# Optimization experiments

Measured on AMD Instinct MI355X. Metric: run time of the kernel, lower is better.

## Reference

```python
import jax, jax.numpy as jnp
import numpy as np

N_HEAD = 8
D_MODEL = 128  # per-head dim == d_model in this 'interpretable' MHA
B, S = 2, 2048
LN_EPS = 1e-3  # keras LayerNormalization default epsilon


def setup_inputs() -> dict:
    key = jax.random.key(0)
    ks = jax.random.split(key, 8)
    sc = 1.0 / np.sqrt(D_MODEL)
    q = jax.random.normal(ks[0], (B, S, D_MODEL), jnp.float32)
    k = jax.random.normal(ks[1], (B, S, D_MODEL), jnp.float32)
    v = jax.random.normal(ks[2], (B, S, D_MODEL), jnp.float32)
    # multiplicative causal mask (lower-triangular ones), broadcast over B,H
    mask = jnp.tril(jnp.ones((S, S), jnp.float32))[None, None, :, :]
    Wq = jax.random.normal(ks[3], (D_MODEL, N_HEAD * D_MODEL), jnp.float32) * sc
    Wk = jax.random.normal(ks[4], (D_MODEL, N_HEAD * D_MODEL), jnp.float32) * sc
    Wv = jax.random.normal(ks[5], (D_MODEL, N_HEAD * D_MODEL), jnp.float32) * sc
    Wo = jax.random.normal(ks[6], (N_HEAD * D_MODEL, D_MODEL), jnp.float32) * sc
    gamma = jnp.ones((D_MODEL,), jnp.float32)
    beta = jnp.zeros((D_MODEL,), jnp.float32)
    return {"q": q, "k": k, "v": v, "mask": mask, "Wq": Wq, "Wk": Wk,
            "Wv": Wv, "Wo": Wo, "gamma": gamma, "beta": beta}


def reference(q, k, v, mask, Wq, Wk, Wv, Wo, gamma, beta):
    b = q.shape[0]
    # projections -> [B, H, S, D]
    def split_heads(x):
        return x.reshape(b, -1, N_HEAD, D_MODEL).transpose(0, 2, 1, 3)
    qs = split_heads(q @ Wq)
    ks_ = split_heads(k @ Wk)
    vs = split_heads(v @ Wv)
    scores = jnp.einsum('bhqd,bhkd->bhqk', qs, ks_) / jnp.sqrt(jnp.float32(D_MODEL))
    scores = scores * mask  # multiplicative mask (NOT additive -inf)
    attn = jax.nn.softmax(scores, axis=-1)
    # dropout layers are identity at inference
    out = jnp.einsum('bhqk,bhkd->bhqd', attn, vs)
    out = out.transpose(0, 2, 1, 3).reshape(b, -1, N_HEAD * D_MODEL)
    out = out @ Wo
    # keras LayerNorm (axis=-1, eps=1e-3)
    mu = jnp.mean(out, axis=-1, keepdims=True)
    var = jnp.var(out, axis=-1, keepdims=True)
    out = (out - mu) * jax.lax.rsqrt(var + LN_EPS) * gamma + beta
    return out
```

## Files before the change

### kernel.cpp

```cpp
#include <hip/hip_runtime.h>
#include <math.h>

#define B 2
#define S 2048
#define H 8
#define D 128
#define DM 1024
#define BH 16

typedef unsigned short u16;
typedef __attribute__((ext_vector_type(8))) short bf16x8;
typedef __attribute__((ext_vector_type(8))) unsigned short u16x8;
typedef __attribute__((ext_vector_type(4))) float f32x4;

__device__ __forceinline__ float bf2f(u16 x) {
    union { unsigned u; float f; } c; c.u = ((unsigned)x) << 16; return c.f;
}
__device__ __forceinline__ u16 f2bf(float f) {
    union { unsigned u; float f; } c; c.f = f;
    unsigned u = c.u; u += 0x7fffu + ((u >> 16) & 1u);
    return (u16)(u >> 16);
}
__device__ __forceinline__ u16 ftr(float f) {
    union { unsigned u; float f; } c; c.f = f;
    return (u16)(c.u >> 16);
}

#define MFMA16(a, b, c) __builtin_amdgcn_mfma_f32_16x16x32_bf16((a), (b), (c), 0, 0, 0)

__global__ __launch_bounds__(256) void prep_kernel(
    const float* __restrict__ Wq, const float* __restrict__ Wk, const float* __restrict__ Wv,
    const float* __restrict__ Wo, u16* __restrict__ WT, u16* __restrict__ WoT)
{
    __shared__ __align__(16) u16 Wl[128][132];
    int tid = threadIdx.x, by = blockIdx.x;
    if (by < 16) {
        int k0 = by * 64;
#pragma unroll
        for (int i = 0; i < 8; i++) {
            int e = i * 256 + tid; int kk = e >> 5, n4 = e & 31;
            float4 w4 = *(const float4*)&Wo[(size_t)(k0 + kk) * D + n4 * 4];
            ushort4 p; p.x = ftr(w4.x); p.y = ftr(w4.y); p.z = ftr(w4.z); p.w = ftr(w4.w);
            *(ushort4*)&Wl[kk][n4 * 4] = p;
        }
        __syncthreads();
#pragma unroll
        for (int i = 0; i < 4; i++) {
            int e = i * 256 + tid; int n = e >> 3, ko = e & 7;
            u16x8 g;
#pragma unroll
            for (int j = 0; j < 8; j++) g[j] = Wl[ko * 8 + j][n];
            *(u16x8*)&WoT[(size_t)n * DM + k0 + ko * 8] = g;
        }
    } else {
        int tile = by - 16;
        int t = tile >> 3, h = tile & 7;
        const float* W = (t == 0) ? Wq : (t == 1) ? Wk : Wv;
        int col0 = h * 128;
#pragma unroll
        for (int i = 0; i < 16; i++) {
            int e = i * 256 + tid; int kk = e >> 5, n4 = e & 31;
            float4 w4 = *(const float4*)&W[(size_t)kk * DM + col0 + n4 * 4];
            ushort4 p; p.x = ftr(w4.x); p.y = ftr(w4.y); p.z = ftr(w4.z); p.w = ftr(w4.w);
            *(ushort4*)&Wl[kk][n4 * 4] = p;
        }
        __syncthreads();
        u16* WTt = WT + (size_t)tile * (128 * 128);
#pragma unroll
        for (int i = 0; i < 8; i++) {
            int e = i * 256 + tid; int n = e >> 4, ko = e & 15;
            u16x8 g;
#pragma unroll
            for (int j = 0; j < 8; j++) g[j] = Wl[ko * 8 + j][n];
            *(u16x8*)&WTt[(size_t)n * 128 + ko * 8] = g;
        }
    }
}

__global__ __launch_bounds__(256) void proj_kernel(
    const float* __restrict__ q, const float* __restrict__ k, const float* __restrict__ v,
    const u16* __restrict__ WT,
    u16* __restrict__ Qo, u16* __restrict__ Ko, u16* __restrict__ VTo,
    float* __restrict__ Csum)
{
    __shared__ __align__(16) u16 Xs[64][136];
    __shared__ __align__(16) u16 Ws[128][136];
    int tid = threadIdx.x;
    int m0 = blockIdx.x * 64;
    int by = blockIdx.y;
    int t = by >> 3;
    int h = by & 7;
    const float* X = (t == 0) ? q : (t == 1) ? k : v;
    const u16* WTt = WT + (size_t)(t * 8 + h) * (128 * 128);

#pragma unroll
    for (int i = 0; i < 8; i++) {
        int e = i * 256 + tid; int r = e >> 5, c4 = e & 31;
        float4 x4 = *(const float4*)&X[(size_t)(m0 + r) * D + c4 * 4];
        ushort4 p; p.x = ftr(x4.x); p.y = ftr(x4.y); p.z = ftr(x4.z); p.w = ftr(x4.w);
        *(ushort4*)&Xs[r][c4 * 4] = p;
    }
#pragma unroll
    for (int i = 0; i < 8; i++) {
        int e = i * 256 + tid; int n = e >> 4, c8 = e & 15;
        *(u16x8*)&Ws[n][c8 * 8] = *(const u16x8*)&WTt[(size_t)n * 128 + c8 * 8];
    }
    __syncthreads();

    int w = tid >> 6, lane = tid & 63, quad = lane >> 4, ln = lane & 15;
    bf16x8 aX[4];
#pragma unroll
    for (int ks = 0; ks < 4; ks++)
        aX[ks] = *(const bf16x8*)&Xs[w * 16 + ln][ks * 32 + quad * 8];

    f32x4 zero = {0.f, 0.f, 0.f, 0.f};
    f32x4 acc[8];
#pragma unroll
    for (int nt = 0; nt < 8; nt++) acc[nt] = zero;

#pragma unroll
    for (int ks = 0; ks < 4; ks++) {
        bf16x8 bW[8];
#pragma unroll
        for (int nt = 0; nt < 8; nt++)
            bW[nt] = *(const bf16x8*)&Ws[nt * 16 + ln][ks * 32 + quad * 8];
#pragma unroll
        for (int nt = 0; nt < 8; nt++)
            acc[nt] = MFMA16(aX[ks], bW[nt], acc[nt]);
    }

    int bb = m0 >> 11, ss0 = m0 & 2047;
    int bh = bb * 8 + h;
    __syncthreads();
    if (t < 2) {
        u16 (*Ct)[136] = Xs;
        u16* O = (t == 0) ? Qo : Ko;
#pragma unroll
        for (int nt = 0; nt < 8; nt++)
#pragma unroll
            for (int r = 0; r < 4; r++)
                Ct[w * 16 + quad * 4 + r][nt * 16 + ln] = f2bf(acc[nt][r]);
        __syncthreads();
#pragma unroll
        for (int i = 0; i < 4; i++) {
            int e = i * 256 + tid; int r = e >> 4, c8 = e & 15;
            *(u16x8*)&O[((size_t)bh * S + ss0 + r) * D + c8 * 8] = *(const u16x8*)&Ct[r][c8 * 8];
        }
    } else {
        u16 (*Ct)[68] = (u16 (*)[68])&Xs[0][0];
#pragma unroll
        for (int nt = 0; nt < 8; nt++)
#pragma unroll
            for (int r = 0; r < 4; r++)
                Ct[nt * 16 + ln][w * 16 + quad * 4 + r] = f2bf(acc[nt][r]);
        __syncthreads();
#pragma unroll
        for (int i = 0; i < 4; i++) {
            int e = i * 256 + tid; int dloc = e >> 3, c8 = e & 7;
            *(u16x8*)&VTo[((size_t)bh * D + dloc) * S + ss0 + c8 * 8] =
                *(const u16x8*)&Ct[dloc][c8 * 8];
        }
        if (tid < 128) {
            int d = tid;
            float s = 0.f;
#pragma unroll
            for (int i = 0; i < 8; i++) {
                u16x8 v8 = *(const u16x8*)&Ct[d][i * 8];
#pragma unroll
                for (int j = 0; j < 8; j++) s += bf2f(v8[j]);
            }
            Csum[((size_t)bh * 32 + (ss0 >> 6)) * D + d] = s;
        }
    }
}

__global__ __launch_bounds__(256, 3) void attn_kernel(
    const u16* __restrict__ Qb, const u16* __restrict__ Kb, const u16* __restrict__ VTg,
    const float* __restrict__ Csum, u16* __restrict__ HOb)
{
    __shared__ __align__(16) u16 Qs[64][136];
    __shared__ __align__(16) u16 Ps[64][72];
    __shared__ __align__(16) u16 Vt[128][72];
    __shared__ float Lred[4][64];

    int tid = threadIdx.x;
    int bh = blockIdx.x;
    int y  = blockIdx.y;
    int qb = (y < 16) ? (31 - y) : (y - 16);
    int q0 = qb * 64;
    int ntile = qb + 1;
    int w = tid >> 6, lane = tid & 63, quad = lane >> 4, ln = lane & 15;
    const u16* Qp  = Qb  + (size_t)bh * S * D;
    const u16* Kp  = Kb  + (size_t)bh * S * D;
    const u16* VTp = VTg + (size_t)bh * D * S;

#pragma unroll
    for (int i = 0; i < 4; i++) {
        int e = i * 256 + tid; int r = e >> 4, c8 = e & 15;
        *(u16x8*)&Qs[r][c8 * 8] = *(const u16x8*)&Qp[(size_t)(q0 + r) * D + c8 * 8];
    }
#pragma unroll
    for (int i = 0; i < 4; i++) {
        int e = i * 256 + tid; int dd = e >> 3, c8 = e & 7;
        *(u16x8*)&Vt[dd][c8 * 8] = *(const u16x8*)&VTp[(size_t)dd * S + c8 * 8];
    }
    bf16x8 kfrag[4];
#pragma unroll
    for (int ks = 0; ks < 4; ks++)
        kfrag[ks] = *(const bf16x8*)&Kp[(size_t)(w * 16 + ln) * D + ks * 32 + quad * 8];
    __syncthreads();

    f32x4 zero = {0.f, 0.f, 0.f, 0.f};
    f32x4 accPV[4][2], acc_l[4];
#pragma unroll
    for (int rf = 0; rf < 4; rf++) { accPV[rf][0] = zero; accPV[rf][1] = zero; acc_l[rf] = zero; }
    bf16x8 bOnes;
#pragma unroll
    for (int j = 0; j < 8; j++) bOnes[j] = (short)0x3F80;
    const float scale = 0.08838834764831845f;

    bf16x8 kn[4];
    u16x8 vreg[4];
    for (int kt = 0; kt < ntile; kt++) {
        int k1 = (kt + 1) * 64;
        bool pf = (kt + 1 < ntile);
        if (pf) {
#pragma unroll
            for (int ks = 0; ks < 4; ks++)
                kn[ks] = *(const bf16x8*)&Kp[(size_t)(k1 + w * 16 + ln) * D + ks * 32 + quad * 8];
#pragma unroll
            for (int i = 0; i < 4; i++) {
                int e = i * 256 + tid; int dd = e >> 3, c8 = e & 7;
                vreg[i] = *(const u16x8*)&VTp[(size_t)dd * S + k1 + c8 * 8];
            }
        }
        f32x4 s[4];
#pragma unroll
        for (int rf = 0; rf < 4; rf++) s[rf] = zero;
        __builtin_amdgcn_s_setprio(1);
#pragma unroll
        for (int ks = 0; ks < 4; ks++) {
#pragma unroll
            for (int rf = 0; rf < 4; rf++) {
                bf16x8 aQ = *(const bf16x8*)&Qs[rf * 16 + ln][ks * 32 + quad * 8];
                s[rf] = MFMA16(aQ, kfrag[ks], s[rf]);
            }
        }
        __builtin_amdgcn_s_setprio(0);
        int colb = kt * 64 + w * 16 + ln;
        if (kt == qb) {
#pragma unroll
            for (int rf = 0; rf < 4; rf++) {
                int rowb = q0 + rf * 16 + quad * 4;
#pragma unroll
                for (int r = 0; r < 4; r++) {
                    float tv = (colb <= rowb + r) ? s[rf][r] : 0.f;
                    Ps[rf * 16 + quad * 4 + r][w * 16 + ln] = f2bf(__expf(tv * scale));
                }
            }
        } else {
#pragma unroll
            for (int rf = 0; rf < 4; rf++)
#pragma unroll
                for (int r = 0; r < 4; r++)
                    Ps[rf * 16 + quad * 4 + r][w * 16 + ln] = f2bf(__expf(s[rf][r] * scale));
        }
        __syncthreads();
        __builtin_amdgcn_s_setprio(1);
#pragma unroll
        for (int ks = 0; ks < 2; ks++) {
            bf16x8 aP[4];
#pragma unroll
            for (int rf = 0; rf < 4; rf++)
                aP[rf] = *(const bf16x8*)&Ps[rf * 16 + ln][ks * 32 + quad * 8];
            bf16x8 v0 = *(const bf16x8*)&Vt[w * 32 + ln][ks * 32 + quad * 8];
            bf16x8 v1 = *(const bf16x8*)&Vt[w * 32 + 16 + ln][ks * 32 + quad * 8];
            if (((kt * 2 + ks) & 3) == w) {
#pragma unroll
                for (int rf = 0; rf < 4; rf++) acc_l[rf] = MFMA16(aP[rf], bOnes, acc_l[rf]);
            }
#pragma unroll
            for (int rf = 0; rf < 4; rf++) {
                accPV[rf][0] = MFMA16(aP[rf], v0, accPV[rf][0]);
                accPV[rf][1] = MFMA16(aP[rf], v1, accPV[rf][1]);
            }
        }
        __builtin_amdgcn_s_setprio(0);
        __syncthreads();
        if (pf) {
#pragma unroll
            for (int i = 0; i < 4; i++) {
                int e = i * 256 + tid; int dd = e >> 3, c8 = e & 7;
                *(u16x8*)&Vt[dd][c8 * 8] = vreg[i];
            }
#pragma unroll
            for (int ks = 0; ks < 4; ks++) kfrag[ks] = kn[ks];
        }
    }

    if (ln == 0) {
#pragma unroll
        for (int rf = 0; rf < 4; rf++)
#pragma unroll
            for (int r = 0; r < 4; r++)
                Lred[w][rf * 16 + quad * 4 + r] = acc_l[rf][r];
    }
    __syncthreads();

    float suf0 = 0.f, suf1 = 0.f;
    for (int c = 31; c >= ntile; c--) {
        const float* cp = &Csum[((size_t)(bh * 32 + c)) * D + w * 32];
        suf0 += cp[ln];
        suf1 += cp[16 + ln];
    }
    int scount = S - ntile * 64;
    int b = bh >> 3, h = bh & 7;
#pragma unroll
    for (int rf = 0; rf < 4; rf++)
#pragma unroll
        for (int r = 0; r < 4; r++) {
            int row = rf * 16 + quad * 4 + r;
            int srow = q0 + row;
            float l = Lred[0][row] + Lred[1][row] + Lred[2][row] + Lred[3][row]
                      + (float)scount;
            float inv = 1.f / l;
            size_t base = ((size_t)(b * S + srow)) * DM + h * D + w * 32;
            HOb[base + ln]      = f2bf((accPV[rf][0][r] + suf0) * inv);
            HOb[base + 16 + ln] = f2bf((accPV[rf][1][r] + suf1) * inv);
        }
}

__global__ __launch_bounds__(256) void out_ln_kernel(
    const u16* __restrict__ HOb, const u16* __restrict__ WoT,
    const float* __restrict__ gamma, const float* __restrict__ beta,
    float* __restrict__ out)
{
    __shared__ __align__(16) u16 HOs[16][1048];
    __shared__ float Cs[16][132];
    int tid = threadIdx.x;
    int m0 = blockIdx.x * 16;
    int w = tid >> 6, lane = tid & 63, quad = lane >> 4, ln = lane & 15;
#pragma unroll
    for (int i = 0; i < 8; i++) {
        int e = i * 256 + tid; int r = e >> 7, c8 = e & 127;
        *(u16x8*)&HOs[r][c8 * 8] = *(const u16x8*)&HOb[(size_t)(m0 + r) * DM + c8 * 8];
    }
    __syncthreads();
    f32x4 zero = {0.f, 0.f, 0.f, 0.f};
    f32x4 acc[2] = {zero, zero};
#pragma unroll 4
    for (int ks = 0; ks < 32; ks++) {
        bf16x8 aH = *(const bf16x8*)&HOs[ln][ks * 32 + quad * 8];
        bf16x8 w0 = *(const bf16x8*)&WoT[(size_t)(w * 32 + ln) * DM + ks * 32 + quad * 8];
        bf16x8 w1 = *(const bf16x8*)&WoT[(size_t)(w * 32 + 16 + ln) * DM + ks * 32 + quad * 8];
        acc[0] = MFMA16(aH, w0, acc[0]);
        acc[1] = MFMA16(aH, w1, acc[1]);
    }
#pragma unroll
    for (int ct = 0; ct < 2; ct++)
#pragma unroll
        for (int r = 0; r < 4; r++)
            Cs[quad * 4 + r][w * 32 + ct * 16 + ln] = acc[ct][r];
    __syncthreads();

    int row = tid >> 4, t16 = tid & 15;
    float xv[8], sum = 0.f, sq = 0.f;
#pragma unroll
    for (int j = 0; j < 8; j++) {
        float x = Cs[row][t16 * 8 + j];
        xv[j] = x; sum += x; sq += x * x;
    }
#pragma unroll
    for (int off = 1; off < 16; off <<= 1) {
        sum += __shfl_xor(sum, off);
        sq  += __shfl_xor(sq, off);
    }
    float mu = sum * (1.f / 128.f);
    float var = sq * (1.f / 128.f) - mu * mu;
    float rstd = rsqrtf(var + 1e-3f);
    float o[8];
#pragma unroll
    for (int j = 0; j < 8; j++) {
        int c = t16 * 8 + j;
        o[j] = (xv[j] - mu) * rstd * gamma[c] + beta[c];
    }
    float* op = &out[(size_t)(m0 + row) * D + t16 * 8];
    *(float4*)&op[0] = *(float4*)&o[0];
    *(float4*)&op[4] = *(float4*)&o[4];
}

extern "C" void kernel_launch(void* const* d_in, const int* in_sizes, int n_in,
                              void* d_out, int out_size, void* d_ws, size_t ws_size,
                              hipStream_t stream)
{
    const float* q     = (const float*)d_in[0];
    const float* k     = (const float*)d_in[1];
    const float* v     = (const float*)d_in[2];
    const float* Wq    = (const float*)d_in[4];
    const float* Wk    = (const float*)d_in[5];
    const float* Wv    = (const float*)d_in[6];
    const float* Wo    = (const float*)d_in[7];
    const float* gamma = (const float*)d_in[8];
    const float* beta  = (const float*)d_in[9];

    u16* ws16 = (u16*)d_ws;
    u16* Qb  = ws16;
    u16* Kb  = ws16 + 4194304;
    u16* VT  = ws16 + 8388608;
    u16* HOb = ws16 + 12582912;
    u16* WoT = ws16 + 16777216;
    u16* WT  = ws16 + 16908288;
    float* Csum = (float*)((char*)d_ws + 35651584);

    prep_kernel<<<40, 256, 0, stream>>>(Wq, Wk, Wv, Wo, WT, WoT);
    proj_kernel<<<dim3(64, 24), 256, 0, stream>>>(q, k, v, WT, Qb, Kb, VT, Csum);
    attn_kernel<<<dim3(BH, 32), 256, 0, stream>>>(Qb, Kb, VT, Csum, HOb);
    out_ln_kernel<<<256, 256, 0, stream>>>(HOb, WoT, gamma, beta, (float*)d_out);
}
```

Baseline: 166.2 us.

## Restructure attention to 512 threads with 128-key tiles and direct V register loads

The attention kernel now runs 8 waves per block and processes 128 keys per iteration. Each wave loads its V fragment directly from global memory into registers instead of staging it through shared memory. The P buffer is double-buffered, which removes the trailing barrier. The diagonal mask is now applied on every tile, and the reordered query-block mapping drops the earlier load-balancing interleave. The aim is fewer synchronisations and fewer LDS round trips, at the cost of masking work on every tile and uncoalesced V reads.

```diff
diff --git a/kernel.cpp b/kernel.cpp
--- a/kernel.cpp
+++ b/kernel.cpp
@@ -174,65 +174,60 @@
     }
 }
 
-__global__ __launch_bounds__(256, 3) void attn_kernel(
+__global__ __launch_bounds__(512, 4) void attn_kernel(
     const u16* __restrict__ Qb, const u16* __restrict__ Kb, const u16* __restrict__ VTg,
     const float* __restrict__ Csum, u16* __restrict__ HOb)
 {
-    __shared__ __align__(16) u16 Qs[64][136];
-    __shared__ __align__(16) u16 Ps[64][72];
-    __shared__ __align__(16) u16 Vt[128][72];
+    __shared__ __align__(16) u16 Qs[64][132];
+    __shared__ __align__(16) u16 Ps[2][64][132];
     __shared__ float Lred[4][64];
 
     int tid = threadIdx.x;
     int bh = blockIdx.x;
     int y  = blockIdx.y;
-    int qb = (y < 16) ? (31 - y) : (y - 16);
+    int qb = 31 - y;
     int q0 = qb * 64;
-    int ntile = qb + 1;
+    int ntile = (qb >> 1) + 1;
     int w = tid >> 6, lane = tid & 63, quad = lane >> 4, ln = lane & 15;
     const u16* Qp  = Qb  + (size_t)bh * S * D;
     const u16* Kp  = Kb  + (size_t)bh * S * D;
     const u16* VTp = VTg + (size_t)bh * D * S;
 
 #pragma unroll
-    for (int i = 0; i < 4; i++) {
-        int e = i * 256 + tid; int r = e >> 4, c8 = e & 15;
+    for (int i = 0; i < 2; i++) {
+        int e = i * 512 + tid; int r = e >> 4, c8 = e & 15;
         *(u16x8*)&Qs[r][c8 * 8] = *(const u16x8*)&Qp[(size_t)(q0 + r) * D + c8 * 8];
     }
-#pragma unroll
-    for (int i = 0; i < 4; i++) {
-        int e = i * 256 + tid; int dd = e >> 3, c8 = e & 7;
-        *(u16x8*)&Vt[dd][c8 * 8] = *(const u16x8*)&VTp[(size_t)dd * S + c8 * 8];
-    }
+    const u16* krow = &Kp[(size_t)(w * 16 + ln) * D + quad * 8];
+    const u16* vrow = &VTp[(size_t)(w * 16 + ln) * S + quad * 8];
     bf16x8 kfrag[4];
 #pragma unroll
     for (int ks = 0; ks < 4; ks++)
-        kfrag[ks] = *(const bf16x8*)&Kp[(size_t)(w * 16 + ln) * D + ks * 32 + quad * 8];
+        kfrag[ks] = *(const bf16x8*)&krow[ks * 32];
     __syncthreads();
 
     f32x4 zero = {0.f, 0.f, 0.f, 0.f};
-    f32x4 accPV[4][2], acc_l[4];
-#pragma unroll
-    for (int rf = 0; rf < 4; rf++) { accPV[rf][0] = zero; accPV[rf][1] = zero; acc_l[rf] = zero; }
+    f32x4 accPV[4], acc_l[4];
+#pragma unroll
+    for (int rf = 0; rf < 4; rf++) { accPV[rf] = zero; acc_l[rf] = zero; }
     bf16x8 bOnes;
 #pragma unroll
     for (int j = 0; j < 8; j++) bOnes[j] = (short)0x3F80;
     const float scale = 0.08838834764831845f;
 
-    bf16x8 kn[4];
-    u16x8 vreg[4];
+    int p = 0;
     for (int kt = 0; kt < ntile; kt++) {
-        int k1 = (kt + 1) * 64;
+        int k0 = kt * 128;
         bool pf = (kt + 1 < ntile);
+        bf16x8 vb[4];
+#pragma unroll
+        for (int ks = 0; ks < 4; ks++)
+            vb[ks] = *(const bf16x8*)&vrow[k0 + ks * 32];
+        bf16x8 kn[4];
         if (pf) {
 #pragma unroll
             for (int ks = 0; ks < 4; ks++)
-                kn[ks] = *(const bf16x8*)&Kp[(size_t)(k1 + w * 16 + ln) * D + ks * 32 + quad * 8];
-#pragma unroll
-            for (int i = 0; i < 4; i++) {
-                int e = i * 256 + tid; int dd = e >> 3, c8 = e & 7;
-                vreg[i] = *(const u16x8*)&VTp[(size_t)dd * S + k1 + c8 * 8];
-            }
+                kn[ks] = *(const bf16x8*)&krow[(size_t)(k0 + 128) * D + ks * 32];
         }
         f32x4 s[4];
 #pragma unroll
@@ -247,58 +242,41 @@
             }
         }
         __builtin_amdgcn_s_setprio(0);
-        int colb = kt * 64 + w * 16 + ln;
-        if (kt == qb) {
-#pragma unroll
-            for (int rf = 0; rf < 4; rf++) {
-                int rowb = q0 + rf * 16 + quad * 4;
-#pragma unroll
-                for (int r = 0; r < 4; r++) {
-                    float tv = (colb <= rowb + r) ? s[rf][r] : 0.f;
-                    Ps[rf * 16 + quad * 4 + r][w * 16 + ln] = f2bf(__expf(tv * scale));
-                }
+        int colb = k0 + w * 16 + ln;
+#pragma unroll
+        for (int rf = 0; rf < 4; rf++) {
+            int rowb = q0 + rf * 16 + quad * 4;
+#pragma unroll
+            for (int r = 0; r < 4; r++) {
+                float tv = (colb <= rowb + r) ? s[rf][r] : 0.f;
+                Ps[p][rf * 16 + quad * 4 + r][w * 16 + ln] = f2bf(__expf(tv * scale));
             }
-        } else {
+        }
+        __syncthreads();
+        __builtin_amdgcn_s_setprio(1);
+#pragma unroll
+        for (int ks = 0; ks < 4; ks++) {
+            bf16x8 aP[4];
 #pragma unroll
             for (int rf = 0; rf < 4; rf++)
-#pragma unroll
-                for (int r = 0; r < 4; r++)
-                    Ps[rf * 16 + quad * 4 + r][w * 16 + ln] = f2bf(__expf(s[rf][r] * scale));
-        }
-        __syncthreads();
-        __builtin_amdgcn_s_setprio(1);
-#pragma unroll
-        for (int ks = 0; ks < 2; ks++) {
-            bf16x8 aP[4];
-#pragma unroll
-            for (int rf = 0; rf < 4; rf++)
-                aP[rf] = *(const bf16x8*)&Ps[rf * 16 + ln][ks * 32 + quad * 8];
-            bf16x8 v0 = *(const bf16x8*)&Vt[w * 32 + ln][ks * 32 + quad * 8];
-            bf16x8 v1 = *(const bf16x8*)&Vt[w * 32 + 16 + ln][ks * 32 + quad * 8];
-            if (((kt * 2 + ks) & 3) == w) {
+                aP[rf] = *(const bf16x8*)&Ps[p][rf * 16 + ln][ks * 32 + quad * 8];
+            if (w < 4 && ks == w) {
 #pragma unroll
                 for (int rf = 0; rf < 4; rf++) acc_l[rf] = MFMA16(aP[rf], bOnes, acc_l[rf]);
             }
 #pragma unroll
-            for (int rf = 0; rf < 4; rf++) {
-                accPV[rf][0] = MFMA16(aP[rf], v0, accPV[rf][0]);
-                accPV[rf][1] = MFMA16(aP[rf], v1, accPV[rf][1]);
-            }
+            for (int rf = 0; rf < 4; rf++)
+                accPV[rf] = MFMA16(aP[rf], vb[ks], accPV[rf]);
         }
         __builtin_amdgcn_s_setprio(0);
-        __syncthreads();
         if (pf) {
 #pragma unroll
-            for (int i = 0; i < 4; i++) {
-                int e = i * 256 + tid; int dd = e >> 3, c8 = e & 7;
-                *(u16x8*)&Vt[dd][c8 * 8] = vreg[i];
-            }
-#pragma unroll
             for (int ks = 0; ks < 4; ks++) kfrag[ks] = kn[ks];
         }
-    }
-
-    if (ln == 0) {
+        p ^= 1;
+    }
+
+    if (w < 4 && ln == 0) {
 #pragma unroll
         for (int rf = 0; rf < 4; rf++)
 #pragma unroll
@@ -307,13 +285,11 @@
     }
     __syncthreads();
 
-    float suf0 = 0.f, suf1 = 0.f;
-    for (int c = 31; c >= ntile; c--) {
-        const float* cp = &Csum[((size_t)(bh * 32 + c)) * D + w * 32];
-        suf0 += cp[ln];
-        suf1 += cp[16 + ln];
-    }
-    int scount = S - ntile * 64;
+    int nt64 = 2 * ntile;
+    float suf = 0.f;
+    for (int c = 31; c >= nt64; c--)
+        suf += Csum[((size_t)(bh * 32 + c)) * D + w * 16 + ln];
+    int scount = S - ntile * 128;
     int b = bh >> 3, h = bh & 7;
 #pragma unroll
     for (int rf = 0; rf < 4; rf++)
@@ -324,9 +300,8 @@
             float l = Lred[0][row] + Lred[1][row] + Lred[2][row] + Lred[3][row]
                       + (float)scount;
             float inv = 1.f / l;
-            size_t base = ((size_t)(b * S + srow)) * DM + h * D + w * 32;
-            HOb[base + ln]      = f2bf((accPV[rf][0][r] + suf0) * inv);
-            HOb[base + 16 + ln] = f2bf((accPV[rf][1][r] + suf1) * inv);
+            HOb[((size_t)(b * S + srow)) * DM + h * D + w * 16 + ln] =
+                f2bf((accPV[rf][r] + suf) * inv);
         }
 }
 
@@ -414,6 +389,6 @@
 
     prep_kernel<<<40, 256, 0, stream>>>(Wq, Wk, Wv, Wo, WT, WoT);
     proj_kernel<<<dim3(64, 24), 256, 0, stream>>>(q, k, v, WT, Qb, Kb, VT, Csum);
-    attn_kernel<<<dim3(BH, 32), 256, 0, stream>>>(Qb, Kb, VT, Csum, HOb);
+    attn_kernel<<<dim3(BH, 32), 512, 0, stream>>>(Qb, Kb, VT, Csum, HOb);
     out_ln_kernel<<<256, 256, 0, stream>>>(HOb, WoT, gamma, beta, (float*)d_out);
 }
```

Result: no change. 165.6 us (-0.4%).

## Stream K/V tiles directly into swizzled LDS with async global_load_lds

Applied to the files above, without the earlier changes.

The attention loop now fetches K and V tiles with global_load_lds straight into XOR-swizzled shared memory. K is double-buffered and Q fragments are held in registers, replacing the old register-staged K fragments and the VGPR-to-LDS copies of V. Synchronisation becomes manual vmcnt waits plus raw barriers, occupancy drops from 3 to 2 blocks per CU, and the interleaved query-block ordering is replaced by a simple descending order. The aim is to cut register pressure and copy instructions and to overlap loads with MFMA work, at the cost of lower occupancy and fragile hand-placed wait counts.

```diff
diff --git a/kernel.cpp b/kernel.cpp
--- a/kernel.cpp
+++ b/kernel.cpp
@@ -27,6 +27,12 @@
 }
 
 #define MFMA16(a, b, c) __builtin_amdgcn_mfma_f32_16x16x32_bf16((a), (b), (c), 0, 0, 0)
+
+__device__ __forceinline__ void gload_lds16(const void* g, void* l) {
+    __builtin_amdgcn_global_load_lds(
+        (__attribute__((address_space(1))) void*)(unsigned long long)(g),
+        (__attribute__((address_space(3))) void*)(unsigned long long)(l), 16, 0, 0);
+}
 
 __global__ __launch_bounds__(256) void prep_kernel(
     const float* __restrict__ Wq, const float* __restrict__ Wk, const float* __restrict__ Wv,
@@ -174,19 +180,19 @@
     }
 }
 
-__global__ __launch_bounds__(256, 3) void attn_kernel(
+__global__ __launch_bounds__(256, 2) void attn_kernel(
     const u16* __restrict__ Qb, const u16* __restrict__ Kb, const u16* __restrict__ VTg,
     const float* __restrict__ Csum, u16* __restrict__ HOb)
 {
-    __shared__ __align__(16) u16 Qs[64][136];
-    __shared__ __align__(16) u16 Ps[64][72];
-    __shared__ __align__(16) u16 Vt[128][72];
+    __shared__ __align__(16) u16 Ks[2][64][128];
+    __shared__ __align__(16) u16 Vt[128][64];
+    __shared__ __align__(16) u16 Ps[64][68];
     __shared__ float Lred[4][64];
 
     int tid = threadIdx.x;
     int bh = blockIdx.x;
     int y  = blockIdx.y;
-    int qb = (y < 16) ? (31 - y) : (y - 16);
+    int qb = 31 - y;
     int q0 = qb * 64;
     int ntile = qb + 1;
     int w = tid >> 6, lane = tid & 63, quad = lane >> 4, ln = lane & 15;
@@ -196,19 +202,39 @@
 
 #pragma unroll
     for (int i = 0; i < 4; i++) {
-        int e = i * 256 + tid; int r = e >> 4, c8 = e & 15;
-        *(u16x8*)&Qs[r][c8 * 8] = *(const u16x8*)&Qp[(size_t)(q0 + r) * D + c8 * 8];
+        int ci = i * 256 + tid;
+        int r = ci >> 4, c = ci & 15;
+        int sc = c ^ (r & 7);
+        gload_lds16(&Qp[(size_t)(q0 + r) * D + sc * 8], (u16*)&Ks[1][0][0] + ci * 8);
     }
 #pragma unroll
     for (int i = 0; i < 4; i++) {
-        int e = i * 256 + tid; int dd = e >> 3, c8 = e & 7;
-        *(u16x8*)&Vt[dd][c8 * 8] = *(const u16x8*)&VTp[(size_t)dd * S + c8 * 8];
-    }
-    bf16x8 kfrag[4];
-#pragma unroll
-    for (int ks = 0; ks < 4; ks++)
-        kfrag[ks] = *(const bf16x8*)&Kp[(size_t)(w * 16 + ln) * D + ks * 32 + quad * 8];
-    __syncthreads();
+        int ci = i * 256 + tid;
+        int r = ci >> 4, c = ci & 15;
+        int sc = c ^ (r & 7);
+        gload_lds16(&Kp[(size_t)r * D + sc * 8], (u16*)&Ks[0][0][0] + ci * 8);
+    }
+    asm volatile("s_waitcnt vmcnt(4)" ::: "memory");
+    __builtin_amdgcn_sched_barrier(0);
+    __builtin_amdgcn_s_barrier();
+    bf16x8 aQ[4][4];
+#pragma unroll
+    for (int rf = 0; rf < 4; rf++)
+#pragma unroll
+        for (int ks = 0; ks < 4; ks++) {
+            int R = rf * 16 + ln;
+            aQ[rf][ks] = *(const bf16x8*)&Ks[1][R][((ks * 4 + quad) ^ (R & 7)) * 8];
+        }
+    asm volatile("s_waitcnt vmcnt(0) lgkmcnt(0)" ::: "memory");
+    __builtin_amdgcn_sched_barrier(0);
+    __builtin_amdgcn_s_barrier();
+#pragma unroll
+    for (int i = 0; i < 4; i++) {
+        int ci = i * 256 + tid;
+        int dd = ci >> 3, c = ci & 7;
+        int sc = c ^ (dd & 7);
+        gload_lds16(&VTp[(size_t)dd * S + sc * 8], (u16*)&Vt[0][0] + ci * 8);
+    }
 
     f32x4 zero = {0.f, 0.f, 0.f, 0.f};
     f32x4 accPV[4][2], acc_l[4];
@@ -219,19 +245,18 @@
     for (int j = 0; j < 8; j++) bOnes[j] = (short)0x3F80;
     const float scale = 0.08838834764831845f;
 
-    bf16x8 kn[4];
-    u16x8 vreg[4];
     for (int kt = 0; kt < ntile; kt++) {
-        int k1 = (kt + 1) * 64;
+        int cur = kt & 1, nxt = cur ^ 1;
+        int k0 = kt * 64;
         bool pf = (kt + 1 < ntile);
         if (pf) {
 #pragma unroll
-            for (int ks = 0; ks < 4; ks++)
-                kn[ks] = *(const bf16x8*)&Kp[(size_t)(k1 + w * 16 + ln) * D + ks * 32 + quad * 8];
-#pragma unroll
             for (int i = 0; i < 4; i++) {
-                int e = i * 256 + tid; int dd = e >> 3, c8 = e & 7;
-                vreg[i] = *(const u16x8*)&VTp[(size_t)dd * S + k1 + c8 * 8];
+                int ci = i * 256 + tid;
+                int r = ci >> 4, c = ci & 15;
+                int sc = c ^ (r & 7);
+                gload_lds16(&Kp[(size_t)(k0 + 64 + r) * D + sc * 8],
+                            (u16*)&Ks[nxt][0][0] + ci * 8);
             }
         }
         f32x4 s[4];
@@ -240,32 +265,27 @@
         __builtin_amdgcn_s_setprio(1);
 #pragma unroll
         for (int ks = 0; ks < 4; ks++) {
-#pragma unroll
-            for (int rf = 0; rf < 4; rf++) {
-                bf16x8 aQ = *(const bf16x8*)&Qs[rf * 16 + ln][ks * 32 + quad * 8];
-                s[rf] = MFMA16(aQ, kfrag[ks], s[rf]);
-            }
+            int R = w * 16 + ln;
+            bf16x8 bK = *(const bf16x8*)&Ks[cur][R][((ks * 4 + quad) ^ (R & 7)) * 8];
+#pragma unroll
+            for (int rf = 0; rf < 4; rf++)
+                s[rf] = MFMA16(aQ[rf][ks], bK, s[rf]);
         }
         __builtin_amdgcn_s_setprio(0);
-        int colb = kt * 64 + w * 16 + ln;
-        if (kt == qb) {
-#pragma unroll
-            for (int rf = 0; rf < 4; rf++) {
-                int rowb = q0 + rf * 16 + quad * 4;
-#pragma unroll
-                for (int r = 0; r < 4; r++) {
-                    float tv = (colb <= rowb + r) ? s[rf][r] : 0.f;
-                    Ps[rf * 16 + quad * 4 + r][w * 16 + ln] = f2bf(__expf(tv * scale));
-                }
-            }
-        } else {
-#pragma unroll
-            for (int rf = 0; rf < 4; rf++)
-#pragma unroll
-                for (int r = 0; r < 4; r++)
-                    Ps[rf * 16 + quad * 4 + r][w * 16 + ln] = f2bf(__expf(s[rf][r] * scale));
-        }
-        __syncthreads();
+        int colb = k0 + w * 16 + ln;
+#pragma unroll
+        for (int rf = 0; rf < 4; rf++) {
+            int rowb = q0 + rf * 16 + quad * 4;
+#pragma unroll
+            for (int r = 0; r < 4; r++) {
+                float tv = (colb <= rowb + r) ? s[rf][r] : 0.f;
+                Ps[rf * 16 + quad * 4 + r][w * 16 + ln] = f2bf(__expf(tv * scale));
+            }
+        }
+        if (pf) asm volatile("s_waitcnt vmcnt(4) lgkmcnt(0)" ::: "memory");
+        else    asm volatile("s_waitcnt vmcnt(0) lgkmcnt(0)" ::: "memory");
+        __builtin_amdgcn_sched_barrier(0);
+        __builtin_amdgcn_s_barrier();
         __builtin_amdgcn_s_setprio(1);
 #pragma unroll
         for (int ks = 0; ks < 2; ks++) {
@@ -273,8 +293,9 @@
 #pragma unroll
             for (int rf = 0; rf < 4; rf++)
                 aP[rf] = *(const bf16x8*)&Ps[rf * 16 + ln][ks * 32 + quad * 8];
-            bf16x8 v0 = *(const bf16x8*)&Vt[w * 32 + ln][ks * 32 + quad * 8];
-            bf16x8 v1 = *(const bf16x8*)&Vt[w * 32 + 16 + ln][ks * 32 + quad * 8];
+            int rv0 = w * 32 + ln, rv1 = w * 32 + 16 + ln;
+            bf16x8 v0 = *(const bf16x8*)&Vt[rv0][((ks * 4 + quad) ^ (rv0 & 7)) * 8];
+            bf16x8 v1 = *(const bf16x8*)&Vt[rv1][((ks * 4 + quad) ^ (rv1 & 7)) * 8];
             if (((kt * 2 + ks) & 3) == w) {
 #pragma unroll
                 for (int rf = 0; rf < 4; rf++) acc_l[rf] = MFMA16(aP[rf], bOnes, acc_l[rf]);
@@ -286,18 +307,21 @@
             }
         }
         __builtin_amdgcn_s_setprio(0);
-        __syncthreads();
+        asm volatile("s_waitcnt vmcnt(0) lgkmcnt(0)" ::: "memory");
+        __builtin_amdgcn_sched_barrier(0);
+        __builtin_amdgcn_s_barrier();
         if (pf) {
 #pragma unroll
             for (int i = 0; i < 4; i++) {
-                int e = i * 256 + tid; int dd = e >> 3, c8 = e & 7;
-                *(u16x8*)&Vt[dd][c8 * 8] = vreg[i];
-            }
-#pragma unroll
-            for (int ks = 0; ks < 4; ks++) kfrag[ks] = kn[ks];
-        }
-    }
-
+                int ci = i * 256 + tid;
+                int dd = ci >> 3, c = ci & 7;
+                int sc = c ^ (dd & 7);
+                gload_lds16(&VTp[(size_t)dd * S + k0 + 64 + sc * 8], (u16*)&Vt[0][0] + ci * 8);
+            }
+        }
+    }
+
+    __syncthreads();
     if (ln == 0) {
 #pragma unroll
         for (int rf = 0; rf < 4; rf++)
```

After: 154.8 us. -6.8%, faster.
